# Optimization experiments

Measured on AMD Instinct MI355X. Metric: run time of the kernel, lower is better.

Reference implementation:

```python
import jax, jax.numpy as jnp
import numpy as np

NEG_INF = -1.0e9  # matches torch masked_fill value


def setup_inputs() -> dict:
    key = jax.random.key(0)
    k1, k2 = jax.random.split(key)
    bs, seq_len, emb_dim = 8, 4096, 512
    max_num_patches = 1024
    h = jax.random.normal(k1, (bs, seq_len, emb_dim), dtype=jnp.float32)
    patch_ids = jnp.sort(
        jax.random.randint(k2, (bs, seq_len), 0, max_num_patches), axis=-1
    )
    return {"h": h, "patch_ids": patch_ids,
            "max_num_patches": max_num_patches, "k": 2}


def reference(h, patch_ids, max_num_patches, k):
    """topk_mean pooling: for each patch (segment) and embedding dim, average
    the top-k values of h among tokens belonging to that patch. Patches with
    fewer than k tokens average only the available tokens; empty patches -> 0.
    Faithful to the torch scatter_reduce(amax)+mask loop."""
    bs, seq_len, emb_dim = h.shape
    b_idx = jnp.arange(bs)[:, None]  # [bs,1] broadcast with patch_ids [bs,seq]
    # tokens-per-patch counts (equivalent of one_hot.sum(dim=1))
    counts = jnp.zeros((bs, max_num_patches), h.dtype).at[b_idx, patch_ids].add(1.0)

    h_work = h
    collected = []
    for _ in range(k):  # k is a small static constant (default 2)
        # segmented amax over tokens -> [bs, P, E]; empty patches get 0
        # (torch scatter_reduce with include_self=False on a zeros base)
        scattered = (jnp.full((bs, max_num_patches, emb_dim), -jnp.inf, h.dtype)
                     .at[b_idx, patch_ids].max(h_work))
        current_max = jnp.where(counts[:, :, None] > 0, scattered, jnp.zeros((), h.dtype))
        collected.append(current_max)
        # gather per-token patch max and mask out positions equal to it
        cur_exp = current_max[b_idx, patch_ids]  # [bs, seq, E]
        h_work = jnp.where(h_work == cur_exp, jnp.asarray(NEG_INF, h.dtype), h_work)

    topk_vals = jnp.stack(collected, axis=2)  # [bs, P, k, E]
    valid = (jnp.arange(k)[None, None, :] < counts[:, :, None]).astype(h.dtype)  # [bs,P,k]
    sum_valid = (topk_vals * valid[..., None]).sum(axis=2)          # [bs, P, E]
    num_valid = jnp.clip(valid.sum(axis=2), 1.0, None)              # [bs, P]
    return sum_valid / num_valid[..., None]
```

## Files before the change

### kernel.cpp

```cpp
#include <hip/hip_runtime.h>


#define NEG_INF (-1.0e9f)

__global__ __launch_bounds__(256) void seg_bounds(
    const int* __restrict__ pid,
    const int* __restrict__ d_P,
    int*       __restrict__ bnd,
    int bs_seq, int pairs)
{
    const int P   = *d_P;
    const int bs  = pairs / P;
    const int seq = bs_seq / bs;

    const int pair = blockIdx.x * blockDim.x + threadIdx.x;
    if (pair >= pairs) return;
    const int b = pair / P;
    const int p = pair - b * P;
    const int* row = pid + (size_t)b * seq;
    int lo = 0, hi = seq;
    while (lo < hi) {
        const int mid = (lo + hi) >> 1;
        if (row[mid] < p) lo = mid + 1; else hi = mid;
    }
    bnd[pair] = lo;
}

__global__ __launch_bounds__(128) void topk_mean_pool(
    const float* __restrict__ h,
    const int*   __restrict__ bnd,
    const int*   __restrict__ d_P,
    const int*   __restrict__ d_k,
    float*       __restrict__ out,
    int bs_seq, int pairs, int E)
{
    const int P   = *d_P;
    const int bs  = pairs / P;
    const int seq = bs_seq / bs;
    const int kk  = *d_k;

    const int pair = blockIdx.x;
    const int b    = pair / P;
    const int p    = pair - b * P;

    const int start = bnd[pair];
    const int end   = (p == P - 1) ? seq : bnd[pair + 1];
    const int n     = end - start;

    const int Ed4 = E >> 2;
    const float4* hb   = (const float4*)h + (size_t)b * seq * Ed4;
    float4*       out4 = (float4*)out + (size_t)pair * Ed4;

    for (int c = threadIdx.x; c < Ed4; c += blockDim.x) {
        float4 r;
        if (n == 0) {
            r = make_float4(0.f, 0.f, 0.f, 0.f);
        } else {
            float4 m1 = make_float4(-INFINITY, -INFINITY, -INFINITY, -INFINITY);
            float4 m2 = m1;
            float4 v = hb[(size_t)start * Ed4 + c];
            for (int t = start; t < end; ++t) {
                float4 vn = v;
                const int tn = t + 1;
                if (tn < end) vn = hb[(size_t)tn * Ed4 + c];
                if (v.x > m1.x) { m2.x = m1.x; m1.x = v.x; }
                else if (v.x < m1.x && v.x > m2.x) { m2.x = v.x; }
                if (v.y > m1.y) { m2.y = m1.y; m1.y = v.y; }
                else if (v.y < m1.y && v.y > m2.y) { m2.y = v.y; }
                if (v.z > m1.z) { m2.z = m1.z; m1.z = v.z; }
                else if (v.z < m1.z && v.z > m2.z) { m2.z = v.z; }
                if (v.w > m1.w) { m2.w = m1.w; m1.w = v.w; }
                else if (v.w < m1.w && v.w > m2.w) { m2.w = v.w; }
                v = vn;
            }
            if (n == 1 || kk == 1) {
                r = m1;
            } else {
                r.x = 0.5f * (m1.x + fmaxf(m2.x, NEG_INF));
                r.y = 0.5f * (m1.y + fmaxf(m2.y, NEG_INF));
                r.z = 0.5f * (m1.z + fmaxf(m2.z, NEG_INF));
                r.w = 0.5f * (m1.w + fmaxf(m2.w, NEG_INF));
            }
        }
        out4[c] = r;
    }
}

extern "C" void kernel_launch(void* const* d_in, const int* in_sizes, int n_in,
                              void* d_out, int out_size, void* d_ws, size_t ws_size,
                              hipStream_t stream) {
    const float* h   = (const float*)d_in[0];
    const int*   pid = (const int*)d_in[1];
    const int*   d_P = (const int*)d_in[2];
    const int*   d_k = (const int*)d_in[3];
    float*       out = (float*)d_out;
    int*         bnd = (int*)d_ws;

    const int h_elems = in_sizes[0];
    const int bs_seq  = in_sizes[1];
    const int E       = h_elems / bs_seq;
    const int pairs   = out_size / E;

    {
        dim3 grid((pairs + 255) / 256), block(256);
        seg_bounds<<<grid, block, 0, stream>>>(pid, d_P, bnd, bs_seq, pairs);
    }
    {
        dim3 grid(pairs), block(128);
        topk_mean_pool<<<grid, block, 0, stream>>>(h, bnd, d_P, d_k, out,
                                                   bs_seq, pairs, E);
    }
}
```

Baseline: 108.3 us.

## Fuse segment-bound search into pooling kernel and process groups of patches per block

Removes the separate binary-search kernel and computes patch boundaries inside the pooling kernel, with each block handling G=4 consecutive patches via shared-memory bounds. Tokens are streamed through a single contiguous scan with D=8 loads issued ahead to increase memory-level parallelism, finalizing each patch as its boundary is crossed. This saves one launch and gives longer contiguous reads per block, at the cost of more control flow inside the inner loop and a quarter as many blocks.

```diff
diff --git a/kernel.cpp b/kernel.cpp
--- a/kernel.cpp
+++ b/kernel.cpp
@@ -2,33 +2,12 @@
 
 
 #define NEG_INF (-1.0e9f)
+#define G 4
+#define D 8
 
-__global__ __launch_bounds__(256) void seg_bounds(
-    const int* __restrict__ pid,
-    const int* __restrict__ d_P,
-    int*       __restrict__ bnd,
-    int bs_seq, int pairs)
-{
-    const int P   = *d_P;
-    const int bs  = pairs / P;
-    const int seq = bs_seq / bs;
-
-    const int pair = blockIdx.x * blockDim.x + threadIdx.x;
-    if (pair >= pairs) return;
-    const int b = pair / P;
-    const int p = pair - b * P;
-    const int* row = pid + (size_t)b * seq;
-    int lo = 0, hi = seq;
-    while (lo < hi) {
-        const int mid = (lo + hi) >> 1;
-        if (row[mid] < p) lo = mid + 1; else hi = mid;
-    }
-    bnd[pair] = lo;
-}
-
-__global__ __launch_bounds__(128) void topk_mean_pool(
+__global__ __launch_bounds__(128) void topk_mean_pool_fused(
     const float* __restrict__ h,
-    const int*   __restrict__ bnd,
+    const int*   __restrict__ pid,
     const int*   __restrict__ d_P,
     const int*   __restrict__ d_k,
     float*       __restrict__ out,
@@ -38,51 +17,93 @@
     const int bs  = pairs / P;
     const int seq = bs_seq / bs;
     const int kk  = *d_k;
+    const int Ed4 = E >> 2;
 
-    const int pair = blockIdx.x;
-    const int b    = pair / P;
-    const int p    = pair - b * P;
+    const int nblk  = (P + G - 1) / G;
+    const int slots = bs * nblk;
 
-    const int start = bnd[pair];
-    const int end   = (p == P - 1) ? seq : bnd[pair + 1];
-    const int n     = end - start;
+    __shared__ int sbd[G + 1];
 
-    const int Ed4 = E >> 2;
-    const float4* hb   = (const float4*)h + (size_t)b * seq * Ed4;
-    float4*       out4 = (float4*)out + (size_t)pair * Ed4;
+    for (int slot = blockIdx.x; slot < slots; slot += gridDim.x) {
+        const int b     = slot / nblk;
+        const int g     = slot - b * nblk;
+        const int p0    = g * G;
+        const int count = min(G, P - p0);
 
-    for (int c = threadIdx.x; c < Ed4; c += blockDim.x) {
-        float4 r;
-        if (n == 0) {
-            r = make_float4(0.f, 0.f, 0.f, 0.f);
-        } else {
+        if (threadIdx.x <= G) {
+            const int  tgt = p0 + (int)threadIdx.x;
+            const int* row = pid + (size_t)b * seq;
+            int lo = 0, hi = seq;
+            while (lo < hi) {
+                const int mid = (lo + hi) >> 1;
+                if (row[mid] < tgt) lo = mid + 1; else hi = mid;
+            }
+            sbd[threadIdx.x] = lo;
+        }
+        __syncthreads();
+
+        const float4* hb   = (const float4*)h + (size_t)b * seq * Ed4;
+        float4*       outb = (float4*)out + (size_t)(b * P + p0) * Ed4;
+
+        for (int c = threadIdx.x; c < Ed4; c += blockDim.x) {
+            const int s  = sbd[0];
+            const int en = sbd[count];
+            int    cur    = 0;
+            int    pstart = s;
+            int    pend   = sbd[1];
             float4 m1 = make_float4(-INFINITY, -INFINITY, -INFINITY, -INFINITY);
             float4 m2 = m1;
-            float4 v = hb[(size_t)start * Ed4 + c];
-            for (int t = start; t < end; ++t) {
-                float4 vn = v;
-                const int tn = t + 1;
-                if (tn < end) vn = hb[(size_t)tn * Ed4 + c];
-                if (v.x > m1.x) { m2.x = m1.x; m1.x = v.x; }
-                else if (v.x < m1.x && v.x > m2.x) { m2.x = v.x; }
-                if (v.y > m1.y) { m2.y = m1.y; m1.y = v.y; }
-                else if (v.y < m1.y && v.y > m2.y) { m2.y = v.y; }
-                if (v.z > m1.z) { m2.z = m1.z; m1.z = v.z; }
-                else if (v.z < m1.z && v.z > m2.z) { m2.z = v.z; }
-                if (v.w > m1.w) { m2.w = m1.w; m1.w = v.w; }
-                else if (v.w < m1.w && v.w > m2.w) { m2.w = v.w; }
-                v = vn;
-            }
-            if (n == 1 || kk == 1) {
-                r = m1;
-            } else {
-                r.x = 0.5f * (m1.x + fmaxf(m2.x, NEG_INF));
-                r.y = 0.5f * (m1.y + fmaxf(m2.y, NEG_INF));
-                r.z = 0.5f * (m1.z + fmaxf(m2.z, NEG_INF));
-                r.w = 0.5f * (m1.w + fmaxf(m2.w, NEG_INF));
+
+            auto finalize = [&]() {
+                const int n = pend - pstart;
+                float4 r;
+                if (n == 0) {
+                    r = make_float4(0.f, 0.f, 0.f, 0.f);
+                } else if (n == 1 || kk == 1) {
+                    r = m1;
+                } else {
+                    r.x = 0.5f * (m1.x + fmaxf(m2.x, NEG_INF));
+                    r.y = 0.5f * (m1.y + fmaxf(m2.y, NEG_INF));
+                    r.z = 0.5f * (m1.z + fmaxf(m2.z, NEG_INF));
+                    r.w = 0.5f * (m1.w + fmaxf(m2.w, NEG_INF));
+                }
+                outb[(size_t)cur * Ed4 + c] = r;
+                m1 = make_float4(-INFINITY, -INFINITY, -INFINITY, -INFINITY);
+                m2 = m1;
+                pstart = pend;
+                ++cur;
+                pend = (cur < count) ? sbd[cur + 1] : 0x7fffffff;
+            };
+
+            while (cur < count && pend == s) finalize();
+
+            int t = s;
+            while (t < en) {
+                const int nload = min(D, en - t);
+                float4 v[D];
+#pragma unroll
+                for (int d = 0; d < D; ++d)
+                    if (d < nload) v[d] = hb[(size_t)(t + d) * Ed4 + c];
+#pragma unroll
+                for (int d = 0; d < D; ++d) {
+                    if (d < nload) {
+                        const float4 vv = v[d];
+                        if (vv.x > m1.x) { m2.x = m1.x; m1.x = vv.x; }
+                        else if (vv.x < m1.x && vv.x > m2.x) { m2.x = vv.x; }
+                        if (vv.y > m1.y) { m2.y = m1.y; m1.y = vv.y; }
+                        else if (vv.y < m1.y && vv.y > m2.y) { m2.y = vv.y; }
+                        if (vv.z > m1.z) { m2.z = m1.z; m1.z = vv.z; }
+                        else if (vv.z < m1.z && vv.z > m2.z) { m2.z = vv.z; }
+                        if (vv.w > m1.w) { m2.w = m1.w; m1.w = vv.w; }
+                        else if (vv.w < m1.w && vv.w > m2.w) { m2.w = vv.w; }
+                        const int tn = t + d + 1;
+                        while (cur < count && pend == tn) finalize();
+                    }
+                }
+                t += nload;
             }
         }
-        out4[c] = r;
+        __syncthreads();
     }
 }
 
@@ -94,20 +115,14 @@
     const int*   d_P = (const int*)d_in[2];
     const int*   d_k = (const int*)d_in[3];
     float*       out = (float*)d_out;
-    int*         bnd = (int*)d_ws;
+    (void)d_ws; (void)ws_size; (void)n_in;
 
     const int h_elems = in_sizes[0];
     const int bs_seq  = in_sizes[1];
     const int E       = h_elems / bs_seq;
     const int pairs   = out_size / E;
 
-    {
-        dim3 grid((pairs + 255) / 256), block(256);
-        seg_bounds<<<grid, block, 0, stream>>>(pid, d_P, bnd, bs_seq, pairs);
-    }
-    {
-        dim3 grid(pairs), block(128);
-        topk_mean_pool<<<grid, block, 0, stream>>>(h, bnd, d_P, d_k, out,
-                                                   bs_seq, pairs, E);
-    }
+    const int grid = (pairs + G - 1) / G;
+    topk_mean_pool_fused<<<dim3(grid), dim3(128), 0, stream>>>(
+        h, pid, d_P, d_k, out, bs_seq, pairs, E);
 }
```

Result: slower. 116.9 us (+7.9%).
